# Kernel optimization log

Hardware: AMD Instinct MI355X
Metric: run time of the kernel (lower is better)

Reference implementation:

```python
import jax, jax.numpy as jnp
import numpy as np

N_NODES = 100000
N_EDGES = 1600000
HIDDEN = 256
CONV_OUT = 128
OUT = 2


def setup_inputs() -> dict:
    key = jax.random.key(0)
    k1, k2, k3, k4, k5, k6, k7 = jax.random.split(key, 7)
    x = jax.random.normal(k1, (N_NODES, HIDDEN), dtype=jnp.float32)
    edge_index = jax.random.randint(k2, (2, N_EDGES), 0, N_NODES, dtype=jnp.int64)
    edge_weight = jax.random.uniform(k3, (N_EDGES,), dtype=jnp.float32)
    # GCNConv parameters (lin: hidden->128, bias added after aggregation)
    W1 = jax.random.normal(k4, (HIDDEN, CONV_OUT), dtype=jnp.float32) / np.sqrt(HIDDEN)
    b1 = jnp.zeros((CONV_OUT,), dtype=jnp.float32)
    # head Linear(128, out_channels)
    W2 = jax.random.normal(k5, (CONV_OUT, OUT), dtype=jnp.float32) / np.sqrt(CONV_OUT)
    b2 = jax.random.normal(k6, (OUT,), dtype=jnp.float32) * 0.01
    return {"x": x, "edge_index": edge_index, "edge_weight": edge_weight,
            "W1": W1, "b1": b1, "W2": W2, "b2": b2}


def reference(x, edge_index, edge_weight, W1, b1, W2, b2):
    # GCNConv (use_weights=True branch, no relu), dropout in eval mode (identity), then Linear.
    N = x.shape[0]
    src, dst = edge_index[0], edge_index[1]
    # add self-loops with weight 1 (PyG default fill_value=1.0)
    loop = jnp.arange(N, dtype=src.dtype)
    src = jnp.concatenate([src, loop])
    dst = jnp.concatenate([dst, loop])
    w = jnp.concatenate([edge_weight, jnp.ones((N,), dtype=edge_weight.dtype)])
    # symmetric normalization: norm = d^{-1/2}[src] * w * d^{-1/2}[dst]
    deg = jax.ops.segment_sum(w, dst, num_segments=N)
    dinv = jnp.where(deg > 0, jax.lax.rsqrt(deg), 0.0)
    norm = dinv[src] * w * dinv[dst]
    # transform then gather-scatter aggregate
    h = x @ W1                                   # [N, 128]
    msgs = norm[:, None] * h[src]                # [E+N, 128]
    agg = jax.ops.segment_sum(msgs, dst, num_segments=N) + b1  # [N, 128]
    return agg @ W2 + b2                         # [N, out_channels]
```

## Files before the change

kernel.cpp:

```cpp
#include <hip/hip_runtime.h>

#define N_NODES 100000
#define N_EDGES 1600000
#define HIDDEN 256

#define BSH 7
#define BNODES 128
#define NB 782
#define NPB 256
#define EPB 6250
#define SLOTS 32
#define NZB 25000


__global__ __launch_bounds__(256) void k_init(
        const float* __restrict__ W1, const float* __restrict__ b1,
        const float* __restrict__ W2, const float* __restrict__ b2,
        float* __restrict__ W12, float* __restrict__ cvec, int* __restrict__ cnt) {
    if (blockIdx.x == 0) {
        int h = threadIdx.x;
        const float4* w1r = (const float4*)(W1 + (size_t)h * 128);
        float a0 = 0.f, a1 = 0.f;
#pragma unroll 8
        for (int k4 = 0; k4 < 32; ++k4) {
            float4 v = w1r[k4];
            a0 += v.x * W2[8 * k4 + 0]; a1 += v.x * W2[8 * k4 + 1];
            a0 += v.y * W2[8 * k4 + 2]; a1 += v.y * W2[8 * k4 + 3];
            a0 += v.z * W2[8 * k4 + 4]; a1 += v.z * W2[8 * k4 + 5];
            a0 += v.w * W2[8 * k4 + 6]; a1 += v.w * W2[8 * k4 + 7];
        }
        W12[2 * h] = a0; W12[2 * h + 1] = a1;
        if (h < 2) {
            float acc = b2[h];
            for (int k = 0; k < 128; ++k) acc += b1[k] * W2[2 * k + h];
            cvec[h] = acc;
        }
    } else {
        int i = (blockIdx.x - 1) * 256 + threadIdx.x;
        if (i < NPB * NB) cnt[i] = 0;
    }
}

__global__ __launch_bounds__(256) void k_z(
        const float* __restrict__ x, const float* __restrict__ W12,
        float* __restrict__ z) {
    const int tid = threadIdx.x;
    const int lane = tid & 63;
    const float2 w0 = ((const float2*)W12)[lane * 4 + 0];
    const float2 w1 = ((const float2*)W12)[lane * 4 + 1];
    const float2 w2 = ((const float2*)W12)[lane * 4 + 2];
    const float2 w3 = ((const float2*)W12)[lane * 4 + 3];
    const int node = blockIdx.x * 4 + (tid >> 6);
    float4 xv = *(const float4*)(x + (size_t)node * HIDDEN + lane * 4);
    float a0 = xv.x * w0.x + xv.y * w1.x + xv.z * w2.x + xv.w * w3.x;
    float a1 = xv.x * w0.y + xv.y * w1.y + xv.z * w2.y + xv.w * w3.y;
#pragma unroll
    for (int m = 32; m >= 1; m >>= 1) {
        a0 += __shfl_xor(a0, m, 64);
        a1 += __shfl_xor(a1, m, 64);
    }
    if (lane == 0) ((float2*)z)[node] = make_float2(a0, a1);
}

__global__ __launch_bounds__(1024) void k_place(
        const int* __restrict__ ei, const float* __restrict__ ew,
        int* __restrict__ cnt, uint2* __restrict__ rec) {
    __shared__ int cursor[NB];
    const int tid = threadIdx.x, bid = blockIdx.x;
    for (int i = tid; i < NB; i += 1024) cursor[i] = 0;
    __syncthreads();
    const int e0 = bid * EPB, e1 = e0 + EPB;
    for (int e = e0 + tid; e < e1; e += 1024) {
        int d = ei[N_EDGES + e];
        int s = ei[e];
        float wv = ew[e];
        int bk = ((unsigned)d) >> BSH;
        int pos = atomicAdd(&cursor[bk], 1);
        if (pos < SLOTS)
            rec[((size_t)bk * NPB + bid) * SLOTS + pos] =
                make_uint2((unsigned)s | ((unsigned)(d & (BNODES - 1)) << 17),
                           __float_as_uint(wv));
    }
    __syncthreads();
    for (int i = tid; i < NB; i += 1024)
        cnt[bid * NB + i] = min(cursor[i], SLOTS);
}

__global__ __launch_bounds__(256) void k_deg(
        const uint2* __restrict__ rec, const int* __restrict__ cnt,
        const float* __restrict__ z, float* __restrict__ dinv,
        float2* __restrict__ zn) {
    __shared__ float acc[BNODES];
    __shared__ int csh[NPB];
    const int tid = threadIdx.x, b = blockIdx.x;
    for (int i = tid; i < BNODES; i += 256) acc[i] = 1.0f;
    csh[tid] = cnt[tid * NB + b];
    __syncthreads();
    const uint2* r = rec + (size_t)b * NPB * SLOTS;
    for (int idx = tid; idx < NPB * SLOTS; idx += 256) {
        int j = idx >> 5, s2 = idx & (SLOTS - 1);
        if (s2 < csh[j]) {
            uint2 q = r[idx];
            atomicAdd(&acc[q.x >> 17], __uint_as_float(q.y));
        }
    }
    __syncthreads();
    for (int i2 = tid; i2 < BNODES; i2 += 256) {
        int node = b * BNODES + i2;
        if (node < N_NODES) {
            float di = rsqrtf(acc[i2]);
            dinv[node] = di;
            float2 zv = ((const float2*)z)[node];
            zn[node] = make_float2(di * zv.x, di * zv.y);
        }
    }
}

__global__ __launch_bounds__(256) void k_gather(
        const uint2* __restrict__ rec, const int* __restrict__ cnt,
        const float* __restrict__ dinv, const float2* __restrict__ zn,
        const float* __restrict__ cvec, float2* __restrict__ out) {
    __shared__ float ax[BNODES], ay[BNODES];
    __shared__ int csh[NPB];
    const int tid = threadIdx.x, b = blockIdx.x;
    for (int i = tid; i < BNODES; i += 256) { ax[i] = 0.f; ay[i] = 0.f; }
    csh[tid] = cnt[tid * NB + b];
    __syncthreads();
    const uint2* r = rec + (size_t)b * NPB * SLOTS;
    for (int idx = tid; idx < NPB * SLOTS; idx += 256) {
        int j = idx >> 5, s2 = idx & (SLOTS - 1);
        if (s2 < csh[j]) {
            uint2 q = r[idx];
            float w = __uint_as_float(q.y);
            float2 s = zn[q.x & 0x1FFFFu];
            int dl = (int)(q.x >> 17);
            atomicAdd(&ax[dl], w * s.x);
            atomicAdd(&ay[dl], w * s.y);
        }
    }
    __syncthreads();
    const float c0 = cvec[0], c1 = cvec[1];
    for (int i2 = tid; i2 < BNODES; i2 += 256) {
        int node = b * BNODES + i2;
        if (node < N_NODES) {
            float di = dinv[node];
            float2 s = zn[node];
            out[node] = make_float2(di * ax[i2] + di * s.x + c0,
                                    di * ay[i2] + di * s.y + c1);
        }
    }
}

extern "C" void kernel_launch(void* const* d_in, const int* in_sizes, int n_in,
                              void* d_out, int out_size, void* d_ws, size_t ws_size,
                              hipStream_t stream) {
    const float* x  = (const float*)d_in[0];
    const int*   ei = (const int*)d_in[1];
    const float* ew = (const float*)d_in[2];
    const float* W1 = (const float*)d_in[3];
    const float* b1 = (const float*)d_in[4];
    const float* W2 = (const float*)d_in[5];
    const float* b2 = (const float*)d_in[6];
    float2* out = (float2*)d_out;

    char* ws = (char*)d_ws;
    uint2*  rec  = (uint2*)ws;           size_t off = (size_t)NB * NPB * SLOTS * 8;
    int*    cnt  = (int*)(ws + off);     off += (size_t)NPB * NB * 4;
    float*  dinv = (float*)(ws + off);   off += (size_t)N_NODES * 4;
    float*  z    = (float*)(ws + off);   off += (size_t)N_NODES * 8;
    float2* zn   = (float2*)(ws + off);  off += (size_t)N_NODES * 8;
    float*  W12  = (float*)(ws + off);   off += HIDDEN * 2 * 4;
    float*  cvec = (float*)(ws + off);   off += 16;

    k_init  <<<1 + (NPB * NB + 255) / 256, 256, 0, stream>>>(W1, b1, W2, b2, W12, cvec, cnt);
    k_z     <<<NZB, 256, 0, stream>>>(x, W12, z);
    k_place <<<NPB, 1024, 0, stream>>>(ei, ew, cnt, rec);
    k_deg   <<<NB, 256, 0, stream>>>(rec, cnt, z, dinv, zn);
    k_gather<<<NB, 256, 0, stream>>>(rec, cnt, dinv, zn, cvec, out);
}
```

Baseline: 85.76 us.

## Fuse z projection and weight folding into degree kernel, drop init and z kernels

Removes the separate init and x·W12 projection kernels. Each degree block now folds W1·W2 into shared memory, projects its own 128 nodes from x, and keeps z in shared memory. The gather kernel computes the folded bias per block. This cuts two launches, the z round trip and the cnt zeroing, but every block redoes the 256×128 weight fold, and the x streaming now runs on only 782 blocks. Skipping the cnt zeroing is safe because k_place writes every cnt entry.

```diff
diff --git a/kernel.cpp b/kernel.cpp
--- a/kernel.cpp
+++ b/kernel.cpp
@@ -10,57 +10,7 @@
 #define NPB 256
 #define EPB 6250
 #define SLOTS 32
-#define NZB 25000
 
-
-__global__ __launch_bounds__(256) void k_init(
-        const float* __restrict__ W1, const float* __restrict__ b1,
-        const float* __restrict__ W2, const float* __restrict__ b2,
-        float* __restrict__ W12, float* __restrict__ cvec, int* __restrict__ cnt) {
-    if (blockIdx.x == 0) {
-        int h = threadIdx.x;
-        const float4* w1r = (const float4*)(W1 + (size_t)h * 128);
-        float a0 = 0.f, a1 = 0.f;
-#pragma unroll 8
-        for (int k4 = 0; k4 < 32; ++k4) {
-            float4 v = w1r[k4];
-            a0 += v.x * W2[8 * k4 + 0]; a1 += v.x * W2[8 * k4 + 1];
-            a0 += v.y * W2[8 * k4 + 2]; a1 += v.y * W2[8 * k4 + 3];
-            a0 += v.z * W2[8 * k4 + 4]; a1 += v.z * W2[8 * k4 + 5];
-            a0 += v.w * W2[8 * k4 + 6]; a1 += v.w * W2[8 * k4 + 7];
-        }
-        W12[2 * h] = a0; W12[2 * h + 1] = a1;
-        if (h < 2) {
-            float acc = b2[h];
-            for (int k = 0; k < 128; ++k) acc += b1[k] * W2[2 * k + h];
-            cvec[h] = acc;
-        }
-    } else {
-        int i = (blockIdx.x - 1) * 256 + threadIdx.x;
-        if (i < NPB * NB) cnt[i] = 0;
-    }
-}
-
-__global__ __launch_bounds__(256) void k_z(
-        const float* __restrict__ x, const float* __restrict__ W12,
-        float* __restrict__ z) {
-    const int tid = threadIdx.x;
-    const int lane = tid & 63;
-    const float2 w0 = ((const float2*)W12)[lane * 4 + 0];
-    const float2 w1 = ((const float2*)W12)[lane * 4 + 1];
-    const float2 w2 = ((const float2*)W12)[lane * 4 + 2];
-    const float2 w3 = ((const float2*)W12)[lane * 4 + 3];
-    const int node = blockIdx.x * 4 + (tid >> 6);
-    float4 xv = *(const float4*)(x + (size_t)node * HIDDEN + lane * 4);
-    float a0 = xv.x * w0.x + xv.y * w1.x + xv.z * w2.x + xv.w * w3.x;
-    float a1 = xv.x * w0.y + xv.y * w1.y + xv.z * w2.y + xv.w * w3.y;
-#pragma unroll
-    for (int m = 32; m >= 1; m >>= 1) {
-        a0 += __shfl_xor(a0, m, 64);
-        a1 += __shfl_xor(a1, m, 64);
-    }
-    if (lane == 0) ((float2*)z)[node] = make_float2(a0, a1);
-}
 
 __global__ __launch_bounds__(1024) void k_place(
         const int* __restrict__ ei, const float* __restrict__ ew,
@@ -86,16 +36,57 @@
         cnt[bid * NB + i] = min(cursor[i], SLOTS);
 }
 
-__global__ __launch_bounds__(256) void k_deg(
+__global__ __launch_bounds__(256) void k_degz(
+        const float* __restrict__ x,
+        const float* __restrict__ W1, const float* __restrict__ W2,
         const uint2* __restrict__ rec, const int* __restrict__ cnt,
-        const float* __restrict__ z, float* __restrict__ dinv,
-        float2* __restrict__ zn) {
+        float* __restrict__ dinv, float2* __restrict__ zn) {
+    __shared__ float w12[HIDDEN * 2];
+    __shared__ float zloc[BNODES][2];
     __shared__ float acc[BNODES];
     __shared__ int csh[NPB];
     const int tid = threadIdx.x, b = blockIdx.x;
+
+    {
+        const float4* w1r = (const float4*)(W1 + (size_t)tid * 128);
+        float a0 = 0.f, a1 = 0.f;
+#pragma unroll 8
+        for (int k4 = 0; k4 < 32; ++k4) {
+            float4 v = w1r[k4];
+            a0 += v.x * W2[8 * k4 + 0]; a1 += v.x * W2[8 * k4 + 1];
+            a0 += v.y * W2[8 * k4 + 2]; a1 += v.y * W2[8 * k4 + 3];
+            a0 += v.z * W2[8 * k4 + 4]; a1 += v.z * W2[8 * k4 + 5];
+            a0 += v.w * W2[8 * k4 + 6]; a1 += v.w * W2[8 * k4 + 7];
+        }
+        w12[2 * tid] = a0; w12[2 * tid + 1] = a1;
+    }
     for (int i = tid; i < BNODES; i += 256) acc[i] = 1.0f;
     csh[tid] = cnt[tid * NB + b];
     __syncthreads();
+
+    const int lane = tid & 63, wv = tid >> 6;
+    const float2 wa = ((const float2*)w12)[lane * 4 + 0];
+    const float2 wb = ((const float2*)w12)[lane * 4 + 1];
+    const float2 wc = ((const float2*)w12)[lane * 4 + 2];
+    const float2 wd = ((const float2*)w12)[lane * 4 + 3];
+    const int base = b * BNODES;
+#pragma unroll 4
+    for (int k = 0; k < 32; ++k) {
+        const int nl = wv * 32 + k;
+        const int node = base + nl;
+        if (node < N_NODES) {
+            float4 xv = *(const float4*)(x + (size_t)node * HIDDEN + lane * 4);
+            float a0 = xv.x * wa.x + xv.y * wb.x + xv.z * wc.x + xv.w * wd.x;
+            float a1 = xv.x * wa.y + xv.y * wb.y + xv.z * wc.y + xv.w * wd.y;
+#pragma unroll
+            for (int m = 32; m >= 1; m >>= 1) {
+                a0 += __shfl_xor(a0, m, 64);
+                a1 += __shfl_xor(a1, m, 64);
+            }
+            if (lane == 0) { zloc[nl][0] = a0; zloc[nl][1] = a1; }
+        }
+    }
+
     const uint2* r = rec + (size_t)b * NPB * SLOTS;
     for (int idx = tid; idx < NPB * SLOTS; idx += 256) {
         int j = idx >> 5, s2 = idx & (SLOTS - 1);
@@ -105,13 +96,13 @@
         }
     }
     __syncthreads();
-    for (int i2 = tid; i2 < BNODES; i2 += 256) {
-        int node = b * BNODES + i2;
+
+    for (int i = tid; i < BNODES; i += 256) {
+        int node = base + i;
         if (node < N_NODES) {
-            float di = rsqrtf(acc[i2]);
+            float di = rsqrtf(acc[i]);
             dinv[node] = di;
-            float2 zv = ((const float2*)z)[node];
-            zn[node] = make_float2(di * zv.x, di * zv.y);
+            zn[node] = make_float2(di * zloc[i][0], di * zloc[i][1]);
         }
     }
 }
@@ -119,12 +110,20 @@
 __global__ __launch_bounds__(256) void k_gather(
         const uint2* __restrict__ rec, const int* __restrict__ cnt,
         const float* __restrict__ dinv, const float2* __restrict__ zn,
-        const float* __restrict__ cvec, float2* __restrict__ out) {
+        const float* __restrict__ b1, const float* __restrict__ W2,
+        const float* __restrict__ b2, float2* __restrict__ out) {
     __shared__ float ax[BNODES], ay[BNODES];
     __shared__ int csh[NPB];
+    __shared__ float cv[2];
     const int tid = threadIdx.x, b = blockIdx.x;
     for (int i = tid; i < BNODES; i += 256) { ax[i] = 0.f; ay[i] = 0.f; }
     csh[tid] = cnt[tid * NB + b];
+    if (tid < 2) {
+        float acc = b2[tid];
+#pragma unroll 8
+        for (int k = 0; k < 128; ++k) acc += b1[k] * W2[2 * k + tid];
+        cv[tid] = acc;
+    }
     __syncthreads();
     const uint2* r = rec + (size_t)b * NPB * SLOTS;
     for (int idx = tid; idx < NPB * SLOTS; idx += 256) {
@@ -139,7 +138,7 @@
         }
     }
     __syncthreads();
-    const float c0 = cvec[0], c1 = cvec[1];
+    const float c0 = cv[0], c1 = cv[1];
     for (int i2 = tid; i2 < BNODES; i2 += 256) {
         int node = b * BNODES + i2;
         if (node < N_NODES) {
@@ -167,14 +166,9 @@
     uint2*  rec  = (uint2*)ws;           size_t off = (size_t)NB * NPB * SLOTS * 8;
     int*    cnt  = (int*)(ws + off);     off += (size_t)NPB * NB * 4;
     float*  dinv = (float*)(ws + off);   off += (size_t)N_NODES * 4;
-    float*  z    = (float*)(ws + off);   off += (size_t)N_NODES * 8;
     float2* zn   = (float2*)(ws + off);  off += (size_t)N_NODES * 8;
-    float*  W12  = (float*)(ws + off);   off += HIDDEN * 2 * 4;
-    float*  cvec = (float*)(ws + off);   off += 16;
 
-    k_init  <<<1 + (NPB * NB + 255) / 256, 256, 0, stream>>>(W1, b1, W2, b2, W12, cvec, cnt);
-    k_z     <<<NZB, 256, 0, stream>>>(x, W12, z);
     k_place <<<NPB, 1024, 0, stream>>>(ei, ew, cnt, rec);
-    k_deg   <<<NB, 256, 0, stream>>>(rec, cnt, z, dinv, zn);
-    k_gather<<<NB, 256, 0, stream>>>(rec, cnt, dinv, zn, cvec, out);
+    k_degz  <<<NB, 256, 0, stream>>>(x, W1, W2, rec, cnt, dinv, zn);
+    k_gather<<<NB, 256, 0, stream>>>(rec, cnt, dinv, zn, b1, W2, b2, out);
 }
```

Result: slower. 101.9 us (+18.8%).

## Fold init into placement kernel, transpose counts, per-thread bucket walks, two nodes per wave

Applied to the files above, without the earlier changes.

Removes the separate init kernel: the W1·W2 fold runs in an extra block of the placement kernel, and zeroing cnt is dropped because placement writes every count. The cnt layout is transposed so each degree/gather thread reads its own source-block slot list and loops only over valid entries, instead of striding over all slots with a predicate. k_z now handles two nodes per wave with one float4 store, halving the block count. The trade-off is per-thread serial loops with uneven lengths and less coalesced reads of rec within a wave.

```diff
diff --git a/kernel.cpp b/kernel.cpp
--- a/kernel.cpp
+++ b/kernel.cpp
@@ -10,63 +10,38 @@
 #define NPB 256
 #define EPB 6250
 #define SLOTS 32
-#define NZB 25000
+#define NZB 12500
 
-
-__global__ __launch_bounds__(256) void k_init(
-        const float* __restrict__ W1, const float* __restrict__ b1,
-        const float* __restrict__ W2, const float* __restrict__ b2,
-        float* __restrict__ W12, float* __restrict__ cvec, int* __restrict__ cnt) {
-    if (blockIdx.x == 0) {
-        int h = threadIdx.x;
-        const float4* w1r = (const float4*)(W1 + (size_t)h * 128);
-        float a0 = 0.f, a1 = 0.f;
-#pragma unroll 8
-        for (int k4 = 0; k4 < 32; ++k4) {
-            float4 v = w1r[k4];
-            a0 += v.x * W2[8 * k4 + 0]; a1 += v.x * W2[8 * k4 + 1];
-            a0 += v.y * W2[8 * k4 + 2]; a1 += v.y * W2[8 * k4 + 3];
-            a0 += v.z * W2[8 * k4 + 4]; a1 += v.z * W2[8 * k4 + 5];
-            a0 += v.w * W2[8 * k4 + 6]; a1 += v.w * W2[8 * k4 + 7];
-        }
-        W12[2 * h] = a0; W12[2 * h + 1] = a1;
-        if (h < 2) {
-            float acc = b2[h];
-            for (int k = 0; k < 128; ++k) acc += b1[k] * W2[2 * k + h];
-            cvec[h] = acc;
-        }
-    } else {
-        int i = (blockIdx.x - 1) * 256 + threadIdx.x;
-        if (i < NPB * NB) cnt[i] = 0;
-    }
-}
-
-__global__ __launch_bounds__(256) void k_z(
-        const float* __restrict__ x, const float* __restrict__ W12,
-        float* __restrict__ z) {
-    const int tid = threadIdx.x;
-    const int lane = tid & 63;
-    const float2 w0 = ((const float2*)W12)[lane * 4 + 0];
-    const float2 w1 = ((const float2*)W12)[lane * 4 + 1];
-    const float2 w2 = ((const float2*)W12)[lane * 4 + 2];
-    const float2 w3 = ((const float2*)W12)[lane * 4 + 3];
-    const int node = blockIdx.x * 4 + (tid >> 6);
-    float4 xv = *(const float4*)(x + (size_t)node * HIDDEN + lane * 4);
-    float a0 = xv.x * w0.x + xv.y * w1.x + xv.z * w2.x + xv.w * w3.x;
-    float a1 = xv.x * w0.y + xv.y * w1.y + xv.z * w2.y + xv.w * w3.y;
-#pragma unroll
-    for (int m = 32; m >= 1; m >>= 1) {
-        a0 += __shfl_xor(a0, m, 64);
-        a1 += __shfl_xor(a1, m, 64);
-    }
-    if (lane == 0) ((float2*)z)[node] = make_float2(a0, a1);
-}
 
 __global__ __launch_bounds__(1024) void k_place(
         const int* __restrict__ ei, const float* __restrict__ ew,
-        int* __restrict__ cnt, uint2* __restrict__ rec) {
+        const float* __restrict__ W1, const float* __restrict__ b1,
+        const float* __restrict__ W2, const float* __restrict__ b2,
+        int* __restrict__ cnt, uint2* __restrict__ rec,
+        float* __restrict__ W12, float* __restrict__ cvec) {
+    const int tid = threadIdx.x, bid = blockIdx.x;
+    if (bid == NPB) {
+        if (tid < HIDDEN) {
+            const float4* w1r = (const float4*)(W1 + (size_t)tid * 128);
+            float a0 = 0.f, a1 = 0.f;
+#pragma unroll 8
+            for (int k4 = 0; k4 < 32; ++k4) {
+                float4 v = w1r[k4];
+                a0 += v.x * W2[8 * k4 + 0]; a1 += v.x * W2[8 * k4 + 1];
+                a0 += v.y * W2[8 * k4 + 2]; a1 += v.y * W2[8 * k4 + 3];
+                a0 += v.z * W2[8 * k4 + 4]; a1 += v.z * W2[8 * k4 + 5];
+                a0 += v.w * W2[8 * k4 + 6]; a1 += v.w * W2[8 * k4 + 7];
+            }
+            W12[2 * tid] = a0; W12[2 * tid + 1] = a1;
+            if (tid < 2) {
+                float acc = b2[tid];
+                for (int k = 0; k < 128; ++k) acc += b1[k] * W2[2 * k + tid];
+                cvec[tid] = acc;
+            }
+        }
+        return;
+    }
     __shared__ int cursor[NB];
-    const int tid = threadIdx.x, bid = blockIdx.x;
     for (int i = tid; i < NB; i += 1024) cursor[i] = 0;
     __syncthreads();
     const int e0 = bid * EPB, e1 = e0 + EPB;
@@ -83,7 +58,32 @@
     }
     __syncthreads();
     for (int i = tid; i < NB; i += 1024)
-        cnt[bid * NB + i] = min(cursor[i], SLOTS);
+        cnt[(size_t)i * NPB + bid] = min(cursor[i], SLOTS);
+}
+
+__global__ __launch_bounds__(256) void k_z(
+        const float* __restrict__ x, const float* __restrict__ W12,
+        float* __restrict__ z) {
+    const int tid = threadIdx.x, lane = tid & 63;
+    const float2 w0 = ((const float2*)W12)[lane * 4 + 0];
+    const float2 w1 = ((const float2*)W12)[lane * 4 + 1];
+    const float2 w2 = ((const float2*)W12)[lane * 4 + 2];
+    const float2 w3 = ((const float2*)W12)[lane * 4 + 3];
+    const int n0 = (blockIdx.x * 4 + (tid >> 6)) * 2;
+    const float4 xa = *(const float4*)(x + (size_t)n0 * HIDDEN + lane * 4);
+    const float4 xb = *(const float4*)(x + (size_t)(n0 + 1) * HIDDEN + lane * 4);
+    float a0 = xa.x * w0.x + xa.y * w1.x + xa.z * w2.x + xa.w * w3.x;
+    float a1 = xa.x * w0.y + xa.y * w1.y + xa.z * w2.y + xa.w * w3.y;
+    float c0 = xb.x * w0.x + xb.y * w1.x + xb.z * w2.x + xb.w * w3.x;
+    float c1 = xb.x * w0.y + xb.y * w1.y + xb.z * w2.y + xb.w * w3.y;
+#pragma unroll
+    for (int m = 32; m >= 1; m >>= 1) {
+        a0 += __shfl_xor(a0, m, 64);
+        a1 += __shfl_xor(a1, m, 64);
+        c0 += __shfl_xor(c0, m, 64);
+        c1 += __shfl_xor(c1, m, 64);
+    }
+    if (lane == 0) *(float4*)(z + 2 * n0) = make_float4(a0, a1, c0, c1);
 }
 
 __global__ __launch_bounds__(256) void k_deg(
@@ -91,24 +91,20 @@
         const float* __restrict__ z, float* __restrict__ dinv,
         float2* __restrict__ zn) {
     __shared__ float acc[BNODES];
-    __shared__ int csh[NPB];
     const int tid = threadIdx.x, b = blockIdx.x;
-    for (int i = tid; i < BNODES; i += 256) acc[i] = 1.0f;
-    csh[tid] = cnt[tid * NB + b];
+    if (tid < BNODES) acc[tid] = 1.0f;
     __syncthreads();
-    const uint2* r = rec + (size_t)b * NPB * SLOTS;
-    for (int idx = tid; idx < NPB * SLOTS; idx += 256) {
-        int j = idx >> 5, s2 = idx & (SLOTS - 1);
-        if (s2 < csh[j]) {
-            uint2 q = r[idx];
-            atomicAdd(&acc[q.x >> 17], __uint_as_float(q.y));
-        }
+    const int n = cnt[(size_t)b * NPB + tid];
+    const uint2* r = rec + ((size_t)b * NPB + tid) * SLOTS;
+    for (int i = 0; i < n; ++i) {
+        uint2 q = r[i];
+        atomicAdd(&acc[q.x >> 17], __uint_as_float(q.y));
     }
     __syncthreads();
-    for (int i2 = tid; i2 < BNODES; i2 += 256) {
-        int node = b * BNODES + i2;
+    if (tid < BNODES) {
+        int node = b * BNODES + tid;
         if (node < N_NODES) {
-            float di = rsqrtf(acc[i2]);
+            float di = rsqrtf(acc[tid]);
             dinv[node] = di;
             float2 zv = ((const float2*)z)[node];
             zn[node] = make_float2(di * zv.x, di * zv.y);
@@ -121,32 +117,27 @@
         const float* __restrict__ dinv, const float2* __restrict__ zn,
         const float* __restrict__ cvec, float2* __restrict__ out) {
     __shared__ float ax[BNODES], ay[BNODES];
-    __shared__ int csh[NPB];
     const int tid = threadIdx.x, b = blockIdx.x;
-    for (int i = tid; i < BNODES; i += 256) { ax[i] = 0.f; ay[i] = 0.f; }
-    csh[tid] = cnt[tid * NB + b];
+    if (tid < BNODES) { ax[tid] = 0.f; ay[tid] = 0.f; }
     __syncthreads();
-    const uint2* r = rec + (size_t)b * NPB * SLOTS;
-    for (int idx = tid; idx < NPB * SLOTS; idx += 256) {
-        int j = idx >> 5, s2 = idx & (SLOTS - 1);
-        if (s2 < csh[j]) {
-            uint2 q = r[idx];
-            float w = __uint_as_float(q.y);
-            float2 s = zn[q.x & 0x1FFFFu];
-            int dl = (int)(q.x >> 17);
-            atomicAdd(&ax[dl], w * s.x);
-            atomicAdd(&ay[dl], w * s.y);
-        }
+    const int n = cnt[(size_t)b * NPB + tid];
+    const uint2* r = rec + ((size_t)b * NPB + tid) * SLOTS;
+    for (int i = 0; i < n; ++i) {
+        uint2 q = r[i];
+        float w = __uint_as_float(q.y);
+        float2 s = zn[q.x & 0x1FFFFu];
+        int dl = (int)(q.x >> 17);
+        atomicAdd(&ax[dl], w * s.x);
+        atomicAdd(&ay[dl], w * s.y);
     }
     __syncthreads();
-    const float c0 = cvec[0], c1 = cvec[1];
-    for (int i2 = tid; i2 < BNODES; i2 += 256) {
-        int node = b * BNODES + i2;
+    if (tid < BNODES) {
+        int node = b * BNODES + tid;
         if (node < N_NODES) {
             float di = dinv[node];
             float2 s = zn[node];
-            out[node] = make_float2(di * ax[i2] + di * s.x + c0,
-                                    di * ay[i2] + di * s.y + c1);
+            out[node] = make_float2(di * ax[tid] + di * s.x + cvec[0],
+                                    di * ay[tid] + di * s.y + cvec[1]);
         }
     }
 }
@@ -165,16 +156,15 @@
 
     char* ws = (char*)d_ws;
     uint2*  rec  = (uint2*)ws;           size_t off = (size_t)NB * NPB * SLOTS * 8;
-    int*    cnt  = (int*)(ws + off);     off += (size_t)NPB * NB * 4;
+    int*    cnt  = (int*)(ws + off);     off += (size_t)NB * NPB * 4;
     float*  dinv = (float*)(ws + off);   off += (size_t)N_NODES * 4;
     float*  z    = (float*)(ws + off);   off += (size_t)N_NODES * 8;
     float2* zn   = (float2*)(ws + off);  off += (size_t)N_NODES * 8;
     float*  W12  = (float*)(ws + off);   off += HIDDEN * 2 * 4;
     float*  cvec = (float*)(ws + off);   off += 16;
 
-    k_init  <<<1 + (NPB * NB + 255) / 256, 256, 0, stream>>>(W1, b1, W2, b2, W12, cvec, cnt);
+    k_place <<<NPB + 1, 1024, 0, stream>>>(ei, ew, W1, b1, W2, b2, cnt, rec, W12, cvec);
     k_z     <<<NZB, 256, 0, stream>>>(x, W12, z);
-    k_place <<<NPB, 1024, 0, stream>>>(ei, ew, cnt, rec);
     k_deg   <<<NB, 256, 0, stream>>>(rec, cnt, z, dinv, zn);
     k_gather<<<NB, 256, 0, stream>>>(rec, cnt, dinv, zn, cvec, out);
 }
```

Measured after the change: 78.65 us. 1.09x faster.
